# Optimization experiments

Hardware: AMD Instinct MI355X
Metric: run time of the kernel (lower is better)

Reference implementation:

```python
import jax, jax.numpy as jnp
import numpy as np

D_MODEL = 1024
N_HEAD = 16
D_K = D_MODEL // N_HEAD


def setup_inputs() -> dict:
    key = jax.random.key(0)
    ks = jax.random.split(key, 11)
    B, S = 2, 2048
    scale = 1.0 / np.sqrt(D_MODEL)
    inp = {
        "q": jax.random.normal(ks[0], (B, S, D_MODEL), jnp.float32),
        "k": jax.random.normal(ks[1], (B, S, D_MODEL), jnp.float32),
        "v": jax.random.normal(ks[2], (B, S, D_MODEL), jnp.float32),
        "Wq": jax.random.normal(ks[3], (D_MODEL, D_MODEL), jnp.float32) * scale,
        "bq": jnp.zeros((D_MODEL,), jnp.float32),
        "Wk": jax.random.normal(ks[4], (D_MODEL, D_MODEL), jnp.float32) * scale,
        "bk": jnp.zeros((D_MODEL,), jnp.float32),
        "Wv": jax.random.normal(ks[5], (D_MODEL, D_MODEL), jnp.float32) * scale,
        "bv": jnp.zeros((D_MODEL,), jnp.float32),
        "Wo": jax.random.normal(ks[6], (D_MODEL, D_MODEL), jnp.float32) * scale,
        "bo": jnp.zeros((D_MODEL,), jnp.float32),
    }
    return inp


def reference(q, k, v, Wq, bq, Wk, bk, Wv, bv, Wo, bo):
    B, S, _ = q.shape
    # QKV projections, split heads: [B, H, S, d_k]
    def proj(x, W, b):
        y = x @ W + b  # [B, S, D]
        return y.reshape(B, -1, N_HEAD, D_K).transpose(0, 2, 1, 3)

    qh = proj(q, Wq, bq)
    kh = proj(k, Wk, bk)
    vh = proj(v, Wv, bv)

    # sigmoid attention (no row normalization)
    scores = jnp.einsum("bhsd,bhtd->bhst", qh, kh) / jnp.sqrt(jnp.float32(D_K))
    attn = jax.nn.sigmoid(scores)  # [B, H, S, S]
    ctx = jnp.einsum("bhst,bhtd->bhsd", attn, vh)

    # merge heads and output projection
    ctx = ctx.transpose(0, 2, 1, 3).reshape(B, S, D_MODEL)
    return ctx @ Wo + bo
```

## Files before the change

kernel.cpp:

```cpp
#include <hip/hip_runtime.h>
#include <stdint.h>
#include <math.h>

typedef _Float16 f16;
typedef _Float16 f16x4 __attribute__((ext_vector_type(4)));
typedef _Float16 f16x8 __attribute__((ext_vector_type(8)));
typedef float f32x4 __attribute__((ext_vector_type(4)));
typedef float f32x16 __attribute__((ext_vector_type(16)));
typedef unsigned int u32;

#define D_MODEL 1024
#define N_HEAD 16
#define BATCH 2
#define SEQ 2048
#define MTOT 4096
#define NQKV 3072
#define QSCALE 0.18033688011112042f

__device__ __forceinline__ void llds16(const void* g, void* l) {
  __builtin_amdgcn_global_load_lds(
      (const __attribute__((address_space(1))) unsigned int*)g,
      (__attribute__((address_space(3))) unsigned int*)l, 16, 0, 0);
}

__device__ __forceinline__ float fast_rcp(float x) {
#if __has_builtin(__builtin_amdgcn_rcpf)
  return __builtin_amdgcn_rcpf(x);
#else
  return 1.0f / x;
#endif
}

__device__ __forceinline__ float fast_exp2(float x) {
#if __has_builtin(__builtin_amdgcn_exp2f)
  return __builtin_amdgcn_exp2f(x);
#else
  return exp2f(x);
#endif
}

#define SIG(s) fast_rcp(1.0f + fast_exp2(-(s)))

__device__ __forceinline__ u32 pk2(float a, float b) {
  auto h = __builtin_amdgcn_cvt_pkrtz(a, b);
  return __builtin_bit_cast(u32, h);
}

__global__ void k_cvt3(const float* __restrict__ q, const float* __restrict__ k,
                       const float* __restrict__ v, f16* __restrict__ dst) {
  const int idx = (blockIdx.x * 256 + threadIdx.x) * 8;
  const int seg = idx >> 22;
  const int off = idx & ((1 << 22) - 1);
  const float* s = (seg == 0) ? q : (seg == 1) ? k : v;
  const float4 a = *(const float4*)(s + off);
  const float4 b = *(const float4*)(s + off + 4);
  f16x8 o;
  o[0] = (f16)a.x; o[1] = (f16)a.y; o[2] = (f16)a.z; o[3] = (f16)a.w;
  o[4] = (f16)b.x; o[5] = (f16)b.y; o[6] = (f16)b.z; o[7] = (f16)b.w;
  *(f16x8*)(dst + idx) = o;
}

__global__ void k_tw(const float* __restrict__ Wq, const float* __restrict__ Wk,
                     const float* __restrict__ Wv, const float* __restrict__ Wo,
                     f16* __restrict__ WqkvT, f16* __restrict__ WoT) {
  __shared__ float t[32][33];
  const int z = blockIdx.z;
  const float* W = (z == 0) ? Wq : (z == 1) ? Wk : (z == 2) ? Wv : Wo;
  f16* dst = (z < 3) ? (WqkvT + (size_t)z * 1024 * 1024) : WoT;
  const int bx = blockIdx.x * 32, by = blockIdx.y * 32;
  const int tx = threadIdx.x, ty = threadIdx.y;
#pragma unroll
  for (int i = 0; i < 32; i += 8)
    t[ty + i][tx] = W[(size_t)(by + ty + i) * 1024 + bx + tx];
  __syncthreads();
#pragma unroll
  for (int i = 0; i < 32; i += 8)
    dst[(size_t)(bx + ty + i) * 1024 + by + tx] = (f16)t[tx][ty + i];
}

template <int Nd, int MODE>
__global__ __launch_bounds__(512, 4) void k_gemm(const f16* __restrict__ A0,
                                                 const f16* __restrict__ A1,
                                                 const f16* __restrict__ A2,
                                                 const f16* __restrict__ BT,
                                                 const float* __restrict__ b0,
                                                 const float* __restrict__ b1,
                                                 const float* __restrict__ b2,
                                                 void* __restrict__ Cout,
                                                 f16* __restrict__ Vt) {
  constexpr int Kd = 1024;
  constexpr int NBX = Nd / 128;
  constexpr int NWG = (MTOT / 128) * NBX;
  __shared__ __align__(16) f16 As[2][8192];
  __shared__ __align__(16) f16 Bs[2][8192];
  int id = blockIdx.x;
  id = (id & 7) * (NWG / 8) + (id >> 3);
  const int n0 = (id % NBX) * 128, m0 = (id / NBX) * 128;
  const f16* A = (Nd == 1024) ? A0 : (n0 < 1024 ? A0 : n0 < 2048 ? A1 : A2);
  const int tid = threadIdx.x, w = tid >> 6, ln = tid & 63;
  const int wm = w >> 2, wn = w & 3;
  f32x4 acc[4][2] = {};

  auto stage = [&](int buf, int kt) {
    const int k0 = kt * 64;
#pragma unroll
    for (int i = 0; i < 2; ++i) {
      const int c = w * 2 + i;
      const int r = c * 8 + (ln >> 3);
      const int g = ln & 7;
      const int ko = k0 + ((g ^ (r & 7)) * 8);
      llds16(A + (size_t)(m0 + r) * Kd + ko, &As[buf][c * 512]);
      llds16(BT + (size_t)(n0 + r) * Kd + ko, &Bs[buf][c * 512]);
    }
  };
  stage(0, 0);
  __syncthreads();
  int cur = 0;
  for (int kt = 0; kt < Kd / 64; ++kt) {
    if (kt < Kd / 64 - 1) stage(cur ^ 1, kt + 1);
#pragma unroll
    for (int kk = 0; kk < 2; ++kk) {
      f16x8 af[4], bf[2];
#pragma unroll
      for (int mi = 0; mi < 4; ++mi) {
        const int r = wm * 64 + mi * 16 + (ln & 15);
        const int g = kk * 4 + (ln >> 4);
        af[mi] = *(const f16x8*)(&As[cur][r * 64 + ((g ^ (r & 7)) * 8)]);
      }
#pragma unroll
      for (int nf = 0; nf < 2; ++nf) {
        const int r = wn * 32 + nf * 16 + (ln & 15);
        const int g = kk * 4 + (ln >> 4);
        bf[nf] = *(const f16x8*)(&Bs[cur][r * 64 + ((g ^ (r & 7)) * 8)]);
      }
#pragma unroll
      for (int mi = 0; mi < 4; ++mi)
#pragma unroll
        for (int nf = 0; nf < 2; ++nf)
          acc[mi][nf] = __builtin_amdgcn_mfma_f32_16x16x32_f16(af[mi], bf[nf], acc[mi][nf], 0, 0, 0);
    }
    __syncthreads();
    cur ^= 1;
  }
  const float* bb = (Nd == 1024) ? b0 : (n0 < 1024 ? b0 : n0 < 2048 ? b1 : b2);
  const int nb = n0 & 1023;
  if (MODE == 0 && n0 >= 2048) {
#pragma unroll
    for (int mi = 0; mi < 4; ++mi)
#pragma unroll
      for (int nf = 0; nf < 2; ++nf) {
        const int cl = wn * 32 + nf * 16 + (ln & 15);
        const int colg = n0 - 2048 + cl;
        const int hd = colg >> 6, d = colg & 63;
        const int row0 = m0 + wm * 64 + mi * 16 + (ln >> 4) * 4;
        const int bI = row0 >> 11, s = row0 & 2047;
        const float bias = bb[nb + cl];
        f16x4 pv;
#pragma unroll
        for (int r = 0; r < 4; ++r) pv[r] = (f16)(acc[mi][nf][r] + bias);
        *(f16x4*)(&Vt[((size_t)(bI * 16 + hd) * 64 + d) * SEQ + s]) = pv;
      }
  } else {
    const float sc = (MODE == 0 && n0 < 1024) ? QSCALE : 1.0f;
#pragma unroll
    for (int mi = 0; mi < 4; ++mi)
#pragma unroll
      for (int nf = 0; nf < 2; ++nf)
#pragma unroll
        for (int r = 0; r < 4; ++r) {
          const int row = m0 + wm * 64 + mi * 16 + (ln >> 4) * 4 + r;
          const int cl = wn * 32 + nf * 16 + (ln & 15);
          const float val = (acc[mi][nf][r] + bb[nb + cl]) * sc;
          if (MODE == 1)
            ((float*)Cout)[(size_t)row * Nd + n0 + cl] = val;
          else
            ((f16*)Cout)[(size_t)row * Nd + n0 + cl] = (f16)val;
        }
  }
}

__global__ __launch_bounds__(256, 2) void k_attn(const f16* __restrict__ QKV,
                                                 const f16* __restrict__ Vt,
                                                 f16* __restrict__ Opart) {
  __shared__ __align__(16) f16 Ks[2][4096];
  __shared__ __align__(16) f16 Vs[2][4096];
  int id = blockIdx.x;
  id = (id & 7) * 128 + (id >> 3);
  const int qt = id & 15, hd = (id >> 4) & 15, b = (id >> 8) & 1, half = id >> 9;
  const int tid = threadIdx.x, w = tid >> 6, ln = tid & 63;
  const int lh = ln >> 5, l31 = ln & 31;
  const int q0 = qt * 128 + w * 32;
  const int kvbase = half * (SEQ / 2);
  const f16* Qb = QKV + ((size_t)b * SEQ) * NQKV + hd * 64;
  const f16* Kb = QKV + ((size_t)b * SEQ) * NQKV + 1024 + hd * 64;
  const f16* Vtb = Vt + (size_t)(b * N_HEAD + hd) * 64 * SEQ;

  f16x8 aq[4];
#pragma unroll
  for (int kk = 0; kk < 4; ++kk)
    aq[kk] = *(const f16x8*)(Qb + (size_t)(q0 + l31) * NQKV + kk * 16 + lh * 8);

  f32x16 oacc0 = {}, oacc1 = {};

  auto stage = [&](int buf, int kt) {
    const int kv0 = kvbase + kt * 64;
#pragma unroll
    for (int i = 0; i < 2; ++i) {
      const int c = w * 2 + i;
      const int r = c * 8 + (ln >> 3);
      const int g = ln & 7;
      llds16(Kb + (size_t)(kv0 + r) * NQKV + ((g ^ (r & 7)) * 8), &Ks[buf][c * 512]);
      llds16(Vtb + (size_t)r * SEQ + kv0 + ((g ^ (r & 7)) * 8), &Vs[buf][c * 512]);
    }
  };
  stage(0, 0);
  __syncthreads();
  int cur = 0;
  for (int kt = 0; kt < SEQ / 128; ++kt) {
    if (kt < SEQ / 128 - 1) stage(cur ^ 1, kt + 1);
    f32x16 sacc0 = {}, sacc1 = {};
#pragma unroll
    for (int kk = 0; kk < 4; ++kk) {
      {
        const int r = l31;
        const f16x8 ak = *(const f16x8*)(&Ks[cur][r * 64 + (((kk * 2 + lh) ^ (r & 7)) * 8)]);
        sacc0 = __builtin_amdgcn_mfma_f32_32x32x16_f16(ak, aq[kk], sacc0, 0, 0, 0);
      }
      {
        const int r = 32 + l31;
        const f16x8 ak = *(const f16x8*)(&Ks[cur][r * 64 + (((kk * 2 + lh) ^ (r & 7)) * 8)]);
        sacc1 = __builtin_amdgcn_mfma_f32_32x32x16_f16(ak, aq[kk], sacc1, 0, 0, 0);
      }
    }
    f16x8 pa[4];
#pragma unroll
    for (int kvt = 0; kvt < 2; ++kvt) {
      const f32x16 sc = kvt ? sacc1 : sacc0;
#pragma unroll
      for (int hf = 0; hf < 2; ++hf) {
        const int b8 = hf * 8;
        u32 X = pk2(SIG(sc[b8 + 0]), SIG(sc[b8 + 1]));
        u32 Y = pk2(SIG(sc[b8 + 2]), SIG(sc[b8 + 3]));
        u32 Z = pk2(SIG(sc[b8 + 4]), SIG(sc[b8 + 5]));
        u32 W = pk2(SIG(sc[b8 + 6]), SIG(sc[b8 + 7]));
        asm volatile("v_permlane32_swap_b32 %0, %1" : "+v"(X), "+v"(Z));
        asm volatile("v_permlane32_swap_b32 %0, %1" : "+v"(Y), "+v"(W));
        union { u32 uw[4]; f16x8 v; } u;
        u.uw[0] = X; u.uw[1] = Y; u.uw[2] = Z; u.uw[3] = W;
        pa[kvt * 2 + hf] = u.v;
      }
    }
#pragma unroll
    for (int c = 0; c < 4; ++c) {
      {
        const int d = l31;
        const f16x8 bv = *(const f16x8*)(&Vs[cur][d * 64 + (((c * 2 + lh) ^ (d & 7)) * 8)]);
        oacc0 = __builtin_amdgcn_mfma_f32_32x32x16_f16(pa[c], bv, oacc0, 0, 0, 0);
      }
      {
        const int d = 32 + l31;
        const f16x8 bv = *(const f16x8*)(&Vs[cur][d * 64 + (((c * 2 + lh) ^ (d & 7)) * 8)]);
        oacc1 = __builtin_amdgcn_mfma_f32_32x32x16_f16(pa[c], bv, oacc1, 0, 0, 0);
      }
    }
    __syncthreads();
    cur ^= 1;
  }
  f16* ob = Opart + (size_t)half * MTOT * D_MODEL;
#pragma unroll
  for (int dt = 0; dt < 2; ++dt) {
    const int dcol = hd * 64 + dt * 32 + l31;
#pragma unroll
    for (int r = 0; r < 16; ++r) {
      const int ql = (r & 3) + 8 * (r >> 2) + 4 * lh;
      const float v = dt ? oacc1[r] : oacc0[r];
      ob[((size_t)b * SEQ + q0 + ql) * D_MODEL + dcol] = (f16)v;
    }
  }
}

__global__ void k_add(const f16* __restrict__ a, const f16* __restrict__ b,
                      f16* __restrict__ o) {
  const int i = (blockIdx.x * 256 + threadIdx.x) * 8;
  const f16x8 x = *(const f16x8*)(a + i);
  const f16x8 y = *(const f16x8*)(b + i);
  f16x8 r;
#pragma unroll
  for (int j = 0; j < 8; ++j) r[j] = (f16)((float)x[j] + (float)y[j]);
  *(f16x8*)(o + i) = r;
}

extern "C" void kernel_launch(void* const* d_in, const int* in_sizes, int n_in,
                              void* d_out, int out_size, void* d_ws, size_t ws_size,
                              hipStream_t stream) {
  (void)in_sizes; (void)n_in; (void)out_size; (void)ws_size;
  const float* q  = (const float*)d_in[0];
  const float* k  = (const float*)d_in[1];
  const float* v  = (const float*)d_in[2];
  const float* Wq = (const float*)d_in[3];
  const float* bq = (const float*)d_in[4];
  const float* Wk = (const float*)d_in[5];
  const float* bk = (const float*)d_in[6];
  const float* Wv = (const float*)d_in[7];
  const float* bv = (const float*)d_in[8];
  const float* Wo = (const float*)d_in[9];
  const float* bo = (const float*)d_in[10];
  float* out = (float*)d_out;

  char* p = (char*)d_ws;
  const size_t SZ_X = (size_t)MTOT * D_MODEL * sizeof(f16);
  f16* qb    = (f16*)p; p += 3 * SZ_X;
  f16* WqkvT = (f16*)p; p += 3 * (size_t)1024 * 1024 * sizeof(f16);
  f16* WoT   = (f16*)p; p += (size_t)1024 * 1024 * sizeof(f16);
  f16* QKVb  = (f16*)p; p += (size_t)MTOT * NQKV * sizeof(f16);
  f16* Vtb   = (f16*)p; p += SZ_X;
  f16* Opart = (f16*)p; p += 2 * SZ_X;
  f16* ctx   = (f16*)p; p += SZ_X;
  f16* kb = qb + (size_t)MTOT * D_MODEL;
  f16* vb = kb + (size_t)MTOT * D_MODEL;

  k_cvt3<<<3 * MTOT * D_MODEL / 2048, 256, 0, stream>>>(q, k, v, qb);
  k_tw<<<dim3(32, 32, 4), dim3(32, 8), 0, stream>>>(Wq, Wk, Wv, Wo, WqkvT, WoT);
  k_gemm<NQKV, 0><<<(MTOT / 128) * (NQKV / 128), 512, 0, stream>>>(
      qb, kb, vb, WqkvT, bq, bk, bv, QKVb, Vtb);
  k_attn<<<(SEQ / 128) * N_HEAD * BATCH * 2, 256, 0, stream>>>(QKVb, Vtb, Opart);
  k_add<<<MTOT * D_MODEL / 2048, 256, 0, stream>>>(
      Opart, Opart + (size_t)MTOT * D_MODEL, ctx);
  k_gemm<1024, 1><<<(MTOT / 128) * (1024 / 128), 512, 0, stream>>>(
      ctx, ctx, ctx, WoT, bo, bo, bo, out, nullptr);
}
```

Baseline: 234.3 us.

## Split attention KV range four ways and prioritize MFMA waves with setprio

```diff
diff --git a/kernel.cpp b/kernel.cpp
--- a/kernel.cpp
+++ b/kernel.cpp
@@ -15,6 +15,7 @@
 #define SEQ 2048
 #define MTOT 4096
 #define NQKV 3072
+#define KVSPLIT 4
 #define QSCALE 0.18033688011112042f
 
 __device__ __forceinline__ void llds16(const void* g, void* l) {
@@ -133,11 +134,13 @@
         const int g = kk * 4 + (ln >> 4);
         bf[nf] = *(const f16x8*)(&Bs[cur][r * 64 + ((g ^ (r & 7)) * 8)]);
       }
+      __builtin_amdgcn_s_setprio(1);
 #pragma unroll
       for (int mi = 0; mi < 4; ++mi)
 #pragma unroll
         for (int nf = 0; nf < 2; ++nf)
           acc[mi][nf] = __builtin_amdgcn_mfma_f32_16x16x32_f16(af[mi], bf[nf], acc[mi][nf], 0, 0, 0);
+      __builtin_amdgcn_s_setprio(0);
     }
     __syncthreads();
     cur ^= 1;
@@ -185,12 +188,12 @@
   __shared__ __align__(16) f16 Ks[2][4096];
   __shared__ __align__(16) f16 Vs[2][4096];
   int id = blockIdx.x;
-  id = (id & 7) * 128 + (id >> 3);
-  const int qt = id & 15, hd = (id >> 4) & 15, b = (id >> 8) & 1, half = id >> 9;
+  id = (id & 7) * 256 + (id >> 3);
+  const int qt = id & 15, hd = (id >> 4) & 15, b = (id >> 8) & 1, qr = id >> 9;
   const int tid = threadIdx.x, w = tid >> 6, ln = tid & 63;
   const int lh = ln >> 5, l31 = ln & 31;
   const int q0 = qt * 128 + w * 32;
-  const int kvbase = half * (SEQ / 2);
+  const int kvbase = qr * (SEQ / KVSPLIT);
   const f16* Qb = QKV + ((size_t)b * SEQ) * NQKV + hd * 64;
   const f16* Kb = QKV + ((size_t)b * SEQ) * NQKV + 1024 + hd * 64;
   const f16* Vtb = Vt + (size_t)(b * N_HEAD + hd) * 64 * SEQ;
@@ -216,9 +219,10 @@
   stage(0, 0);
   __syncthreads();
   int cur = 0;
-  for (int kt = 0; kt < SEQ / 128; ++kt) {
-    if (kt < SEQ / 128 - 1) stage(cur ^ 1, kt + 1);
+  for (int kt = 0; kt < SEQ / KVSPLIT / 64; ++kt) {
+    if (kt < SEQ / KVSPLIT / 64 - 1) stage(cur ^ 1, kt + 1);
     f32x16 sacc0 = {}, sacc1 = {};
+    __builtin_amdgcn_s_setprio(1);
 #pragma unroll
     for (int kk = 0; kk < 4; ++kk) {
       {
@@ -232,6 +236,7 @@
         sacc1 = __builtin_amdgcn_mfma_f32_32x32x16_f16(ak, aq[kk], sacc1, 0, 0, 0);
       }
     }
+    __builtin_amdgcn_s_setprio(0);
     f16x8 pa[4];
 #pragma unroll
     for (int kvt = 0; kvt < 2; ++kvt) {
@@ -250,6 +255,7 @@
         pa[kvt * 2 + hf] = u.v;
       }
     }
+    __builtin_amdgcn_s_setprio(1);
 #pragma unroll
     for (int c = 0; c < 4; ++c) {
       {
@@ -263,10 +269,11 @@
         oacc1 = __builtin_amdgcn_mfma_f32_32x32x16_f16(pa[c], bv, oacc1, 0, 0, 0);
       }
     }
+    __builtin_amdgcn_s_setprio(0);
     __syncthreads();
     cur ^= 1;
   }
-  f16* ob = Opart + (size_t)half * MTOT * D_MODEL;
+  f16* ob = Opart + (size_t)qr * MTOT * D_MODEL;
 #pragma unroll
   for (int dt = 0; dt < 2; ++dt) {
     const int dcol = hd * 64 + dt * 32 + l31;
@@ -279,14 +286,17 @@
   }
 }
 
-__global__ void k_add(const f16* __restrict__ a, const f16* __restrict__ b,
-                      f16* __restrict__ o) {
+__global__ void k_add4(const f16* __restrict__ a, f16* __restrict__ o) {
+  const size_t plane = (size_t)MTOT * D_MODEL;
   const int i = (blockIdx.x * 256 + threadIdx.x) * 8;
-  const f16x8 x = *(const f16x8*)(a + i);
-  const f16x8 y = *(const f16x8*)(b + i);
+  const f16x8 x0 = *(const f16x8*)(a + i);
+  const f16x8 x1 = *(const f16x8*)(a + plane + i);
+  const f16x8 x2 = *(const f16x8*)(a + 2 * plane + i);
+  const f16x8 x3 = *(const f16x8*)(a + 3 * plane + i);
   f16x8 r;
 #pragma unroll
-  for (int j = 0; j < 8; ++j) r[j] = (f16)((float)x[j] + (float)y[j]);
+  for (int j = 0; j < 8; ++j)
+    r[j] = (f16)(((float)x0[j] + (float)x1[j]) + ((float)x2[j] + (float)x3[j]));
   *(f16x8*)(o + i) = r;
 }
 
@@ -314,18 +324,17 @@
   f16* WoT   = (f16*)p; p += (size_t)1024 * 1024 * sizeof(f16);
   f16* QKVb  = (f16*)p; p += (size_t)MTOT * NQKV * sizeof(f16);
   f16* Vtb   = (f16*)p; p += SZ_X;
-  f16* Opart = (f16*)p; p += 2 * SZ_X;
-  f16* ctx   = (f16*)p; p += SZ_X;
+  f16* Opart = (f16*)p; p += KVSPLIT * SZ_X;
   f16* kb = qb + (size_t)MTOT * D_MODEL;
   f16* vb = kb + (size_t)MTOT * D_MODEL;
+  f16* ctx = qb;
 
   k_cvt3<<<3 * MTOT * D_MODEL / 2048, 256, 0, stream>>>(q, k, v, qb);
   k_tw<<<dim3(32, 32, 4), dim3(32, 8), 0, stream>>>(Wq, Wk, Wv, Wo, WqkvT, WoT);
   k_gemm<NQKV, 0><<<(MTOT / 128) * (NQKV / 128), 512, 0, stream>>>(
       qb, kb, vb, WqkvT, bq, bk, bv, QKVb, Vtb);
-  k_attn<<<(SEQ / 128) * N_HEAD * BATCH * 2, 256, 0, stream>>>(QKVb, Vtb, Opart);
-  k_add<<<MTOT * D_MODEL / 2048, 256, 0, stream>>>(
-      Opart, Opart + (size_t)MTOT * D_MODEL, ctx);
+  k_attn<<<(SEQ / 128) * N_HEAD * BATCH * KVSPLIT, 256, 0, stream>>>(QKVb, Vtb, Opart);
+  k_add4<<<MTOT * D_MODEL / 2048, 256, 0, stream>>>(Opart, ctx);
   k_gemm<1024, 1><<<(MTOT / 128) * (1024 / 128), 512, 0, stream>>>(
       ctx, ctx, ctx, WoT, bo, bo, bo, out, nullptr);
 }
```

New measurement: 233.4 us. Within noise of the previous version (-0.4%).

## Use 256x256 tiled QKV GEMM with deeper prefetch pipeline

Applied to the files above, without the earlier changes.

```diff
diff --git a/kernel.cpp b/kernel.cpp
--- a/kernel.cpp
+++ b/kernel.cpp
@@ -78,17 +78,131 @@
     dst[(size_t)(bx + ty + i) * 1024 + by + tx] = (f16)t[tx][ty + i];
 }
 
-template <int Nd, int MODE>
-__global__ __launch_bounds__(512, 4) void k_gemm(const f16* __restrict__ A0,
-                                                 const f16* __restrict__ A1,
-                                                 const f16* __restrict__ A2,
-                                                 const f16* __restrict__ BT,
-                                                 const float* __restrict__ b0,
-                                                 const float* __restrict__ b1,
-                                                 const float* __restrict__ b2,
-                                                 void* __restrict__ Cout,
-                                                 f16* __restrict__ Vt) {
-  constexpr int Kd = 1024;
+__global__ __launch_bounds__(512, 2) void k_gemm256(const f16* __restrict__ A0,
+                                                    const f16* __restrict__ A1,
+                                                    const f16* __restrict__ A2,
+                                                    const f16* __restrict__ BT,
+                                                    const float* __restrict__ b0,
+                                                    const float* __restrict__ b1,
+                                                    const float* __restrict__ b2,
+                                                    f16* __restrict__ Cout,
+                                                    f16* __restrict__ Vt) {
+  constexpr int Kd = 1024, NT = Kd / 64;
+  constexpr int NBX = NQKV / 256;
+  constexpr int NWG = (MTOT / 256) * NBX;
+  __shared__ __align__(16) f16 As[2][256 * 64];
+  __shared__ __align__(16) f16 Bs[2][256 * 64];
+  int id = blockIdx.x;
+  id = (id & 7) * (NWG / 8) + (id >> 3);
+  const int n0 = (id % NBX) * 256, m0 = (id / NBX) * 256;
+  const f16* A = (n0 < 1024) ? A0 : (n0 < 2048 ? A1 : A2);
+  const int tid = threadIdx.x, w = tid >> 6, ln = tid & 63;
+  const int wm = w >> 2, wn = w & 3;
+
+  f32x4 acc[8][4] = {};
+
+  auto stage = [&](int d, int kt) {
+    const int k0 = kt * 64;
+    const int rsub = w * 8 + (ln >> 3);
+    const int gsw = ((ln & 7) ^ (ln >> 3)) * 8;
+#pragma unroll
+    for (int i = 0; i < 4; ++i) {
+      const int r = i * 64 + rsub;
+      llds16(A + (size_t)(m0 + r) * Kd + k0 + gsw, &As[d][(i * 64 + w * 8) * 64]);
+    }
+#pragma unroll
+    for (int i = 0; i < 4; ++i) {
+      const int r = i * 64 + rsub;
+      llds16(BT + (size_t)(n0 + r) * Kd + k0 + gsw, &Bs[d][(i * 64 + w * 8) * 64]);
+    }
+  };
+
+  stage(0, 0);
+  stage(1, 1);
+  for (int t = 0; t < NT; ++t) {
+    const int d = t & 1;
+    if (t + 1 < NT) {
+      asm volatile("s_waitcnt vmcnt(8)" ::: "memory");
+    } else {
+      asm volatile("s_waitcnt vmcnt(0)" ::: "memory");
+    }
+    __builtin_amdgcn_sched_barrier(0);
+    __builtin_amdgcn_s_barrier();
+    __builtin_amdgcn_sched_barrier(0);
+#pragma unroll
+    for (int q = 0; q < 4; ++q) {
+      const int mb = (q & 1) * 4, nb = (q >> 1) * 2;
+      f16x8 af[4][2], bf[2][2];
+#pragma unroll
+      for (int kk = 0; kk < 2; ++kk) {
+        const int g = kk * 4 + (ln >> 4);
+#pragma unroll
+        for (int mi = 0; mi < 4; ++mi) {
+          const int r = wm * 128 + (mb + mi) * 16 + (ln & 15);
+          af[mi][kk] = *(const f16x8*)(&As[d][r * 64 + ((g ^ (r & 7)) * 8)]);
+        }
+#pragma unroll
+        for (int nf = 0; nf < 2; ++nf) {
+          const int r = wn * 64 + (nb + nf) * 16 + (ln & 15);
+          bf[nf][kk] = *(const f16x8*)(&Bs[d][r * 64 + ((g ^ (r & 7)) * 8)]);
+        }
+      }
+      __builtin_amdgcn_s_setprio(1);
+#pragma unroll
+      for (int kk = 0; kk < 2; ++kk)
+#pragma unroll
+        for (int mi = 0; mi < 4; ++mi)
+#pragma unroll
+          for (int nf = 0; nf < 2; ++nf)
+            acc[mb + mi][nb + nf] = __builtin_amdgcn_mfma_f32_16x16x32_f16(
+                af[mi][kk], bf[nf][kk], acc[mb + mi][nb + nf], 0, 0, 0);
+      __builtin_amdgcn_s_setprio(0);
+    }
+    __builtin_amdgcn_sched_barrier(0);
+    __builtin_amdgcn_s_barrier();
+    __builtin_amdgcn_sched_barrier(0);
+    if (t + 2 < NT) stage(d, t + 2);
+  }
+
+  const float* bb = (n0 < 1024) ? b0 : (n0 < 2048 ? b1 : b2);
+  const int nb0 = n0 & 1023;
+  if (n0 >= 2048) {
+#pragma unroll
+    for (int mi = 0; mi < 8; ++mi)
+#pragma unroll
+      for (int nf = 0; nf < 4; ++nf) {
+        const int cl = wn * 64 + nf * 16 + (ln & 15);
+        const int colg = n0 - 2048 + cl;
+        const int hd = colg >> 6, dd = colg & 63;
+        const int row0 = m0 + wm * 128 + mi * 16 + (ln >> 4) * 4;
+        const int bI = row0 >> 11, s = row0 & 2047;
+        const float bias = bb[nb0 + cl];
+        f16x4 pv;
+#pragma unroll
+        for (int r = 0; r < 4; ++r) pv[r] = (f16)(acc[mi][nf][r] + bias);
+        *(f16x4*)(&Vt[((size_t)(bI * 16 + hd) * 64 + dd) * SEQ + s]) = pv;
+      }
+  } else {
+    const float sc = (n0 < 1024) ? QSCALE : 1.0f;
+#pragma unroll
+    for (int mi = 0; mi < 8; ++mi)
+#pragma unroll
+      for (int nf = 0; nf < 4; ++nf)
+#pragma unroll
+        for (int r = 0; r < 4; ++r) {
+          const int row = m0 + wm * 128 + mi * 16 + (ln >> 4) * 4 + r;
+          const int cl = wn * 64 + nf * 16 + (ln & 15);
+          Cout[(size_t)row * NQKV + n0 + cl] =
+              (f16)((acc[mi][nf][r] + bb[nb0 + cl]) * sc);
+        }
+  }
+}
+
+__global__ __launch_bounds__(512, 4) void k_gemmO(const f16* __restrict__ A,
+                                                  const f16* __restrict__ BT,
+                                                  const float* __restrict__ bias,
+                                                  float* __restrict__ Cout) {
+  constexpr int Kd = 1024, Nd = 1024;
   constexpr int NBX = Nd / 128;
   constexpr int NWG = (MTOT / 128) * NBX;
   __shared__ __align__(16) f16 As[2][8192];
@@ -96,7 +210,6 @@
   int id = blockIdx.x;
   id = (id & 7) * (NWG / 8) + (id >> 3);
   const int n0 = (id % NBX) * 128, m0 = (id / NBX) * 128;
-  const f16* A = (Nd == 1024) ? A0 : (n0 < 1024 ? A0 : n0 < 2048 ? A1 : A2);
   const int tid = threadIdx.x, w = tid >> 6, ln = tid & 63;
   const int wm = w >> 2, wn = w & 3;
   f32x4 acc[4][2] = {};
@@ -142,41 +255,16 @@
     __syncthreads();
     cur ^= 1;
   }
-  const float* bb = (Nd == 1024) ? b0 : (n0 < 1024 ? b0 : n0 < 2048 ? b1 : b2);
-  const int nb = n0 & 1023;
-  if (MODE == 0 && n0 >= 2048) {
-#pragma unroll
-    for (int mi = 0; mi < 4; ++mi)
-#pragma unroll
-      for (int nf = 0; nf < 2; ++nf) {
+#pragma unroll
+  for (int mi = 0; mi < 4; ++mi)
+#pragma unroll
+    for (int nf = 0; nf < 2; ++nf)
+#pragma unroll
+      for (int r = 0; r < 4; ++r) {
+        const int row = m0 + wm * 64 + mi * 16 + (ln >> 4) * 4 + r;
         const int cl = wn * 32 + nf * 16 + (ln & 15);
-        const int colg = n0 - 2048 + cl;
-        const int hd = colg >> 6, d = colg & 63;
-        const int row0 = m0 + wm * 64 + mi * 16 + (ln >> 4) * 4;
-        const int bI = row0 >> 11, s = row0 & 2047;
-        const float bias = bb[nb + cl];
-        f16x4 pv;
-#pragma unroll
-        for (int r = 0; r < 4; ++r) pv[r] = (f16)(acc[mi][nf][r] + bias);
-        *(f16x4*)(&Vt[((size_t)(bI * 16 + hd) * 64 + d) * SEQ + s]) = pv;
-      }
-  } else {
-    const float sc = (MODE == 0 && n0 < 1024) ? QSCALE : 1.0f;
-#pragma unroll
-    for (int mi = 0; mi < 4; ++mi)
-#pragma unroll
-      for (int nf = 0; nf < 2; ++nf)
-#pragma unroll
-        for (int r = 0; r < 4; ++r) {
-          const int row = m0 + wm * 64 + mi * 16 + (ln >> 4) * 4 + r;
-          const int cl = wn * 32 + nf * 16 + (ln & 15);
-          const float val = (acc[mi][nf][r] + bb[nb + cl]) * sc;
-          if (MODE == 1)
-            ((float*)Cout)[(size_t)row * Nd + n0 + cl] = val;
-          else
-            ((f16*)Cout)[(size_t)row * Nd + n0 + cl] = (f16)val;
-        }
-  }
+        Cout[(size_t)row * Nd + n0 + cl] = acc[mi][nf][r] + bias[n0 + cl];
+      }
 }
 
 __global__ __launch_bounds__(256, 2) void k_attn(const f16* __restrict__ QKV,
@@ -315,17 +403,16 @@
   f16* QKVb  = (f16*)p; p += (size_t)MTOT * NQKV * sizeof(f16);
   f16* Vtb   = (f16*)p; p += SZ_X;
   f16* Opart = (f16*)p; p += 2 * SZ_X;
-  f16* ctx   = (f16*)p; p += SZ_X;
   f16* kb = qb + (size_t)MTOT * D_MODEL;
   f16* vb = kb + (size_t)MTOT * D_MODEL;
+  f16* ctx = qb;
 
   k_cvt3<<<3 * MTOT * D_MODEL / 2048, 256, 0, stream>>>(q, k, v, qb);
   k_tw<<<dim3(32, 32, 4), dim3(32, 8), 0, stream>>>(Wq, Wk, Wv, Wo, WqkvT, WoT);
-  k_gemm<NQKV, 0><<<(MTOT / 128) * (NQKV / 128), 512, 0, stream>>>(
+  k_gemm256<<<(MTOT / 256) * (NQKV / 256), 512, 0, stream>>>(
       qb, kb, vb, WqkvT, bq, bk, bv, QKVb, Vtb);
   k_attn<<<(SEQ / 128) * N_HEAD * BATCH * 2, 256, 0, stream>>>(QKVb, Vtb, Opart);
   k_add<<<MTOT * D_MODEL / 2048, 256, 0, stream>>>(
       Opart, Opart + (size_t)MTOT * D_MODEL, ctx);
-  k_gemm<1024, 1><<<(MTOT / 128) * (1024 / 128), 512, 0, stream>>>(
-      ctx, ctx, ctx, WoT, bo, bo, bo, out, nullptr);
-}
+  k_gemmO<<<(MTOT / 128) * (1024 / 128), 512, 0, stream>>>(ctx, WoT, bo, out);
+}
```

Result: faster. 228.4 us (-2.5%).
